# Optimization experiments

Hardware: AMD Instinct MI355X
Metric: run time of the kernel (lower is better)

Reference implementation:

```python
import jax, jax.numpy as jnp
import numpy as np

D_MODEL = 2048
N_HEADS = 16
HEAD_DIM = D_MODEL // N_HEADS
SEQ = 2048
THETA = 10000.0


def rope_tables(head_dim, context_length, theta=THETA):
    inv_freq = 1.0 / theta ** (jnp.arange(0, head_dim, 2, dtype=jnp.float32) / head_dim)
    angles = jnp.arange(context_length, dtype=jnp.float32)[:, None] * inv_freq[None, :]
    angles = jnp.concatenate([angles, angles], axis=1)  # [S, head_dim]
    return jnp.cos(angles), jnp.sin(angles)


def apply_rope(x, cos, sin):
    # x: [B, H, S, Dh]; cos/sin: [S, Dh]
    half = x.shape[-1] // 2
    x1, x2 = x[..., :half], x[..., half:]
    rotated = jnp.concatenate([-x2, x1], axis=-1)
    return x * cos[None, None] + rotated * sin[None, None]


def setup_inputs() -> dict:
    key = jax.random.key(0)
    ks = jax.random.split(key, 5)
    s = 1.0 / np.sqrt(D_MODEL)
    x = jax.random.normal(ks[0], (2, SEQ, D_MODEL), dtype=jnp.float32)
    Wq = jax.random.normal(ks[1], (D_MODEL, D_MODEL), dtype=jnp.float32) * s
    Wk = jax.random.normal(ks[2], (D_MODEL, D_MODEL), dtype=jnp.float32) * s
    Wv = jax.random.normal(ks[3], (D_MODEL, D_MODEL), dtype=jnp.float32) * s
    Wo = jax.random.normal(ks[4], (D_MODEL, D_MODEL), dtype=jnp.float32) * s
    return {"x": x, "Wq": Wq, "Wk": Wk, "Wv": Wv, "Wo": Wo}


def reference(x, Wq, Wk, Wv, Wo):
    B, S, D = x.shape
    cos, sin = rope_tables(HEAD_DIM, SEQ)
    cos, sin = cos[:S], sin[:S]

    def split_heads(t):  # [B,S,D] -> [B,H,S,Dh]
        return t.reshape(B, S, N_HEADS, HEAD_DIM).transpose(0, 2, 1, 3)

    q = apply_rope(split_heads(x @ Wq.T), cos, sin)
    k = apply_rope(split_heads(x @ Wk.T), cos, sin)
    v = split_heads(x @ Wv.T)

    scores = jnp.einsum('bhqd,bhkd->bhqk', q, k) / np.sqrt(HEAD_DIM).astype(np.float32)
    causal = jnp.tril(jnp.ones((S, S), dtype=bool))
    scores = jnp.where(causal[None, None], scores, -jnp.inf)
    weights = jax.nn.softmax(scores, axis=-1)
    ctx = jnp.einsum('bhqk,bhkd->bhqd', weights, v)
    ctx = ctx.transpose(0, 2, 1, 3).reshape(B, S, D)
    return ctx @ Wo.T
```

## Files before the change

kernel.cpp:

```cpp
#include <hip/hip_runtime.h>
#include <hip/hip_bf16.h>
#include <cstdint>
#include <cstddef>

typedef __bf16 bf16;
typedef __bf16 bf16x4 __attribute__((ext_vector_type(4)));
typedef __bf16 bf16x8 __attribute__((ext_vector_type(8)));
typedef float f32x4 __attribute__((ext_vector_type(4)));

#define D_MODEL 2048
#define SEQ     2048
#define NH      16
#define HD      128
#define BATCH   2
#define QKV_LD  6144

#define SBAR()  __builtin_amdgcn_sched_barrier(0)
#define HWBAR() do { SBAR(); __builtin_amdgcn_s_barrier(); SBAR(); } while (0)

__device__ __forceinline__ void gld16(void* lds, const void* g) {
    __builtin_amdgcn_global_load_lds(
        (const __attribute__((address_space(1))) unsigned int*)g,
        (__attribute__((address_space(3))) unsigned int*)lds,
        16, 0, 0);
}

__global__ __launch_bounds__(256) void cvt_all(const float* __restrict__ x,
                                               const float* __restrict__ Wq,
                                               const float* __restrict__ Wk,
                                               const float* __restrict__ Wv,
                                               const float* __restrict__ Wo,
                                               bf16* __restrict__ out) {
    int i = (blockIdx.x * 256 + threadIdx.x) * 4;
    const float* src;
    int off;
    if (i < 8388608) { src = x; off = i; }
    else {
        int j = i - 8388608;
        int seg = j >> 22;
        src = (seg == 0) ? Wq : (seg == 1) ? Wk : (seg == 2) ? Wv : Wo;
        off = j & 4194303;
    }
    float4 v = *(const float4*)(src + off);
    bf16* o = out + i;
    o[0] = (bf16)v.x; o[1] = (bf16)v.y; o[2] = (bf16)v.z; o[3] = (bf16)v.w;
}

__global__ __launch_bounds__(256) void rope_tables_k(float* __restrict__ cosd,
                                                     float* __restrict__ sind) {
    int id = blockIdx.x * 256 + threadIdx.x;
    int s = id >> 6, d = id & 63;
    float freq = powf(10000.f, -(float)d * (1.f / 64.f));
    float a = (float)s * freq;
    float sn, c;
    sincosf(a, &sn, &c);
    cosd[id] = c;
    sind[id] = sn;
}

__global__ __launch_bounds__(256) void rope_apply2(bf16* __restrict__ T,
                                                   const float* __restrict__ cosd,
                                                   const float* __restrict__ sind,
                                                   float qscale) {
    int id = blockIdx.x * 256 + threadIdx.x;
    int half = id >> 22;
    int jd = id & 4194303;
    int row = jd >> 10;
    int p = jd & 1023;
    int h = p >> 6, d = p & 63;
    int s = row & (SEQ - 1);
    size_t base = (size_t)row * QKV_LD + half * D_MODEL + h * HD + d;
    float scale = half ? 1.0f : qscale;
    float x1 = (float)T[base];
    float x2 = (float)T[base + 64];
    float c = cosd[(s << 6) + d];
    float sn = sind[(s << 6) + d];
    T[base]      = (bf16)((x1 * c - x2 * sn) * scale);
    T[base + 64] = (bf16)((x2 * c + x1 * sn) * scale);
}

__global__ __launch_bounds__(256) void transpose_v(const bf16* __restrict__ V,
                                                   bf16* __restrict__ Vt, int ld) {
    __shared__ bf16 t[32][33];
    int s0 = blockIdx.x * 32;
    int d0 = blockIdx.y * 32;
    int bh = blockIdx.z;
    int b = bh >> 4, h = bh & 15;
    int tx = threadIdx.x & 31, ty = threadIdx.x >> 5;
#pragma unroll
    for (int i = 0; i < 32; i += 8)
        t[ty + i][tx] = V[((size_t)(b * SEQ + s0 + ty + i)) * ld + h * HD + d0 + tx];
    __syncthreads();
#pragma unroll
    for (int i = 0; i < 32; i += 8)
        Vt[((size_t)bh * HD + d0 + ty + i) * SEQ + s0 + tx] = t[tx][ty + i];
}

template <int OUTF32>
__global__ __launch_bounds__(512, 2)
void gemm128(const bf16* __restrict__ A, const bf16* __restrict__ B,
             void* __restrict__ Cout, int M, int N, int K) {
    __shared__ __align__(16) bf16 ldsA[2][128 * 64];
    __shared__ __align__(16) bf16 ldsB[2][2][128 * 64];

    const int nN = N >> 8;
    const int cpx = gridDim.x >> 3;
    const int lin = (blockIdx.x & 7) * cpx + (blockIdx.x >> 3);
    const int m0 = (lin / nN) * 128, n0 = (lin % nN) * 256;

    const int tid = threadIdx.x;
    const int w = tid >> 6, l = tid & 63;
    const int wm = w >> 2, wn = w & 3;
    const int lg = l >> 4, lc = l & 15;
    const int swz = (lc & 7) << 4;
    const int NT = K >> 6;

    f32x4 acc[2][4][2] = {};

    auto stageA = [&](int tau) {
        bf16* dst = &ldsA[tau & 1][0];
#pragma unroll
        for (int j = 0; j < 2; ++j) {
            int r = w * 16 + j * 8 + (l >> 3);
            int scb = ((l & 7) * 16) ^ ((r & 7) << 4);
            gld16(dst + (w * 16 + j * 8) * 64, A + (size_t)(m0 + r) * K + tau * 64 + (scb >> 1));
        }
    };
    auto stageB = [&](int tau, int u) {
        bf16* dst = &ldsB[tau & 1][u][0];
#pragma unroll
        for (int j = 0; j < 2; ++j) {
            int r = w * 16 + j * 8 + (l >> 3);
            int scb = ((l & 7) * 16) ^ ((r & 7) << 4);
            gld16(dst + (w * 16 + j * 8) * 64, B + (size_t)(n0 + u * 128 + r) * K + tau * 64 + (scb >> 1));
        }
    };

    stageA(0); stageB(0, 0); stageB(0, 1); stageA(1);
    SBAR();
    asm volatile("s_waitcnt vmcnt(2)" ::: "memory");
    HWBAR();

    for (int t = 0; t < NT; ++t) {
        const int c = t & 1;
        const char* Ab = (const char*)&ldsA[c][0];
        const char* Bb = (const char*)&ldsB[c][wn >> 1][0];
        const int brow0 = (wn & 1) * 64;
        bf16x8 Af[4][2], Bf[2][2];

#pragma unroll
        for (int mt = 0; mt < 4; ++mt)
#pragma unroll
            for (int ks = 0; ks < 2; ++ks)
                Af[mt][ks] = *(const bf16x8*)(Ab + (wm * 64 + mt * 16 + lc) * 128 + ((ks * 64 + lg * 16) ^ swz));
#pragma unroll
        for (int nt = 0; nt < 2; ++nt)
#pragma unroll
            for (int ks = 0; ks < 2; ++ks)
                Bf[nt][ks] = *(const bf16x8*)(Bb + (brow0 + nt * 16 + lc) * 128 + ((ks * 64 + lg * 16) ^ swz));
        if (t + 1 < NT) stageB(t + 1, 0);
        HWBAR();
        __builtin_amdgcn_s_setprio(1);
#pragma unroll
        for (int mt = 0; mt < 4; ++mt)
#pragma unroll
            for (int nt = 0; nt < 2; ++nt)
#pragma unroll
                for (int ks = 0; ks < 2; ++ks)
                    acc[0][mt][nt] = __builtin_amdgcn_mfma_f32_16x16x32_bf16(Af[mt][ks], Bf[nt][ks], acc[0][mt][nt], 0, 0, 0);
        __builtin_amdgcn_s_setprio(0);
        HWBAR();

#pragma unroll
        for (int nt = 0; nt < 2; ++nt)
#pragma unroll
            for (int ks = 0; ks < 2; ++ks)
                Bf[nt][ks] = *(const bf16x8*)(Bb + (brow0 + 32 + nt * 16 + lc) * 128 + ((ks * 64 + lg * 16) ^ swz));
        if (t + 1 < NT) stageB(t + 1, 1);
        if (t + 2 < NT) stageA(t + 2);
        HWBAR();
        __builtin_amdgcn_s_setprio(1);
#pragma unroll
        for (int mt = 0; mt < 4; ++mt)
#pragma unroll
            for (int nt = 0; nt < 2; ++nt)
#pragma unroll
                for (int ks = 0; ks < 2; ++ks)
                    acc[1][mt][nt] = __builtin_amdgcn_mfma_f32_16x16x32_bf16(Af[mt][ks], Bf[nt][ks], acc[1][mt][nt], 0, 0, 0);
        __builtin_amdgcn_s_setprio(0);
        SBAR();
        if (t + 2 < NT) asm volatile("s_waitcnt vmcnt(2)" ::: "memory");
        else            asm volatile("s_waitcnt vmcnt(0)" ::: "memory");
        HWBAR();
    }

#pragma unroll
    for (int nq = 0; nq < 2; ++nq)
#pragma unroll
        for (int mt = 0; mt < 4; ++mt)
#pragma unroll
            for (int nt = 0; nt < 2; ++nt)
#pragma unroll
                for (int rr = 0; rr < 4; ++rr) {
                    size_t row = (size_t)m0 + wm * 64 + mt * 16 + lg * 4 + rr;
                    size_t col = (size_t)n0 + wn * 64 + nq * 32 + nt * 16 + lc;
                    float v = acc[nq][mt][nt][rr];
                    if (OUTF32) ((float*)Cout)[row * N + col] = v;
                    else        ((bf16*)Cout)[row * N + col] = (bf16)v;
                }
}

__global__ __launch_bounds__(512)
void flash_attn(const bf16* __restrict__ QKV, const bf16* __restrict__ Vt,
                bf16* __restrict__ O) {
    __shared__ __align__(16) bf16 Ks[2][64 * 128];
    __shared__ __align__(16) bf16 Vs[2][128 * 64];
    __shared__ __align__(16) bf16 p_lds[8][16 * 64];

    const int bid = blockIdx.x;
    const int xcd = bid & 7, loc = bid >> 3;
    const int bh = (xcd << 2) + (loc & 3);
    const int jjj = loc >> 2;
    const int qt = (jjj < 8) ? (15 - jjj) : (jjj - 8);
    const int b = bh >> 4, h = bh & 15;

    const int tid = threadIdx.x;
    const int w = tid >> 6, l = tid & 63;
    const int lg = l >> 4, lc = l & 15;
    const int kswz = (lc & 7) << 4;
    char* pb = (char*)&p_lds[w][0];

    auto stageK = [&](int p, int kb) {
#pragma unroll
        for (int c = 0; c < 2; ++c) {
            int r = c * 32 + w * 4 + (l >> 4);
            int scb = ((l & 15) * 16) ^ ((r & 7) << 4);
            const bf16* g = QKV + ((size_t)(b * SEQ + kb * 64 + r)) * QKV_LD + D_MODEL + h * HD + (scb >> 1);
            gld16(&Ks[p][(c * 32 + w * 4) * 128], g);
        }
    };
    auto stageV = [&](int p, int kb) {
#pragma unroll
        for (int c = 0; c < 2; ++c) {
            int r = c * 64 + w * 8 + (l >> 3);
            int scb = ((l & 7) * 16) ^ ((r & 7) << 4);
            const bf16* g = Vt + ((size_t)bh * HD + r) * SEQ + kb * 64 + (scb >> 1);
            gld16(&Vs[p][(c * 64 + w * 8) * 64], g);
        }
    };

    const int q0 = qt * 128 + w * 16;
    const int kbmax = 2 * qt + 1;

    const bf16* qp = QKV + ((size_t)(b * SEQ + q0 + lc)) * QKV_LD + h * HD + lg * 8;
    bf16x8 qf[4];
#pragma unroll
    for (int kc = 0; kc < 4; ++kc) qf[kc] = *(const bf16x8*)(qp + kc * 32);

    f32x4 ctx[8] = {};
    float m_s = -INFINITY, l_s = 0.f;

    int cur = 0;
    stageK(cur, 0);
    stageV(cur, 0);

    for (int kb = 0; kb <= kbmax; ++kb) {
        __syncthreads();
        if (kb < kbmax) { stageK(cur ^ 1, kb + 1); stageV(cur ^ 1, kb + 1); }

        const char* kbp = (const char*)&Ks[cur][0];
        f32x4 st[4] = {};
#pragma unroll
        for (int nf = 0; nf < 4; ++nf) {
            int krow = nf * 16 + lc;
#pragma unroll
            for (int kc = 0; kc < 4; ++kc) {
                bf16x8 kf = *(const bf16x8*)(kbp + krow * 256 + ((kc * 64 + lg * 16) ^ kswz));
                st[nf] = __builtin_amdgcn_mfma_f32_16x16x32_bf16(kf, qf[kc], st[nf], 0, 0, 0);
            }
        }

        if (kb >= 2 * qt) {
            int q = q0 + lc;
#pragma unroll
            for (int nf = 0; nf < 4; ++nf) {
                int key = kb * 64 + nf * 16 + lg * 4;
#pragma unroll
                for (int r = 0; r < 4; ++r)
                    if (key + r > q) st[nf][r] = -INFINITY;
            }
        }

        float m01 = fmaxf(fmaxf(st[0][0], st[0][1]), fmaxf(st[0][2], st[0][3]));
        float m23 = fmaxf(fmaxf(st[1][0], st[1][1]), fmaxf(st[1][2], st[1][3]));
        float m45 = fmaxf(fmaxf(st[2][0], st[2][1]), fmaxf(st[2][2], st[2][3]));
        float m67 = fmaxf(fmaxf(st[3][0], st[3][1]), fmaxf(st[3][2], st[3][3]));
        float mx = fmaxf(fmaxf(m01, m23), fmaxf(m45, m67));
        mx = fmaxf(mx, __shfl_xor(mx, 16));
        mx = fmaxf(mx, __shfl_xor(mx, 32));

        bool defer = __all(mx <= m_s + 8.f) && (m_s > -INFINITY);
        float mi;
        if (defer) {
            mi = m_s;
        } else {
            mi = fmaxf(m_s, mx);
            float scv = __expf(m_s - mi);
            float scvr[4];
#pragma unroll
            for (int r = 0; r < 4; ++r) scvr[r] = __shfl(scv, lg * 4 + r);
#pragma unroll
            for (int nd = 0; nd < 8; ++nd)
#pragma unroll
                for (int r = 0; r < 4; ++r) ctx[nd][r] *= scvr[r];
            l_s *= scv;
            m_s = mi;
        }

        float rs = 0.f;
#pragma unroll
        for (int nf = 0; nf < 4; ++nf) {
            float p0 = __expf(st[nf][0] - mi);
            float p1 = __expf(st[nf][1] - mi);
            float p2 = __expf(st[nf][2] - mi);
            float p3 = __expf(st[nf][3] - mi);
            rs += (p0 + p1) + (p2 + p3);
            bf16x4 pv = { (bf16)p0, (bf16)p1, (bf16)p2, (bf16)p3 };
            *(bf16x4*)(pb + lc * 128 + ((nf * 32 + lg * 8) ^ kswz)) = pv;
        }
        rs += __shfl_xor(rs, 16);
        rs += __shfl_xor(rs, 32);
        l_s += rs;

        asm volatile("s_waitcnt lgkmcnt(0)" ::: "memory");
        SBAR();
        bf16x8 pa0 = *(const bf16x8*)(pb + lc * 128 + ((lg * 16) ^ kswz));
        bf16x8 pa1 = *(const bf16x8*)(pb + lc * 128 + ((64 + lg * 16) ^ kswz));

        const char* vb = (const char*)&Vs[cur][0];
#pragma unroll
        for (int nd = 0; nd < 8; ++nd) {
            int vrow = nd * 16 + lc;
#pragma unroll
            for (int k2 = 0; k2 < 2; ++k2) {
                bf16x8 vf = *(const bf16x8*)(vb + vrow * 128 + ((k2 * 64 + lg * 16) ^ kswz));
                ctx[nd] = __builtin_amdgcn_mfma_f32_16x16x32_bf16(k2 ? pa1 : pa0, vf, ctx[nd], 0, 0, 0);
            }
        }
        cur ^= 1;
    }

    float lr[4];
#pragma unroll
    for (int r = 0; r < 4; ++r) lr[r] = 1.f / __shfl(l_s, lg * 4 + r);
#pragma unroll
    for (int nd = 0; nd < 8; ++nd)
#pragma unroll
        for (int r = 0; r < 4; ++r)
            O[((size_t)(b * SEQ + q0 + lg * 4 + r)) * D_MODEL + h * HD + nd * 16 + lc] =
                (bf16)(ctx[nd][r] * lr[r]);
}

extern "C" void kernel_launch(void* const* d_in, const int* in_sizes, int n_in,
                              void* d_out, int out_size, void* d_ws, size_t ws_size,
                              hipStream_t stream) {
    const float* x  = (const float*)d_in[0];
    const float* Wq = (const float*)d_in[1];
    const float* Wk = (const float*)d_in[2];
    const float* Wv = (const float*)d_in[3];
    const float* Wo = (const float*)d_in[4];

    char* ws = (char*)d_ws;
    bf16* xb   = (bf16*)(ws + 0);
    bf16* wqkv = (bf16*)(ws + 16777216);
    bf16* wob  = (bf16*)(ws + 41943040);
    bf16* QKV  = (bf16*)(ws + 50331648);
    bf16* Vtb  = (bf16*)(ws + 100663296);
    float* cosd = (float*)(ws + 117440512);
    float* sind = (float*)(ws + 117964800);

    cvt_all<<<25165824 / 1024, 256, 0, stream>>>(x, Wq, Wk, Wv, Wo, xb);

    rope_tables_k<<<(SEQ * 64) / 256, 256, 0, stream>>>(cosd, sind);

    gemm128<0><<<dim3(768), 512, 0, stream>>>(
        xb, wqkv, QKV, BATCH * SEQ, QKV_LD, D_MODEL);

    const float qscale = 0.08838834764831845f;
    rope_apply2<<<(2 * BATCH * SEQ * 1024) / 256, 256, 0, stream>>>(QKV, cosd, sind, qscale);

    transpose_v<<<dim3(SEQ / 32, HD / 32, BATCH * NH), 256, 0, stream>>>(QKV + 2 * D_MODEL, Vtb, QKV_LD);

    flash_attn<<<dim3(512), 512, 0, stream>>>(QKV, Vtb, xb );

    gemm128<1><<<dim3(256), 512, 0, stream>>>(
        xb, wob, d_out, BATCH * SEQ, D_MODEL, D_MODEL);
}
```

Before: 269.1 us.

## Use 256x256 tiled GEMM with quadrant-split pipeline for QKV projection

```diff
diff --git a/kernel.cpp b/kernel.cpp
--- a/kernel.cpp
+++ b/kernel.cpp
@@ -98,6 +98,147 @@
 
 template <int OUTF32>
 __global__ __launch_bounds__(512, 2)
+void gemm256(const bf16* __restrict__ A, const bf16* __restrict__ B,
+             void* __restrict__ Cout, int M, int N, int K) {
+    __shared__ __align__(16) bf16 lds[2][2][2][128 * 64];
+
+    const int nN = N >> 8;
+    const int cpx = gridDim.x >> 3;
+    const int lin = (blockIdx.x & 7) * cpx + (blockIdx.x >> 3);
+    const int m0 = (lin / nN) * 256, n0 = (lin % nN) * 256;
+
+    const int tid = threadIdx.x;
+    const int w = tid >> 6, l = tid & 63;
+    const int wm = w >> 2, wn = w & 3;
+    const int lg = l >> 4, lc = l & 15;
+    const int swz = (lc & 7) << 4;
+    const int NT = K >> 6;
+
+    f32x4 acc[2][2][4][2] = {};
+
+    auto stage = [&](int tau, int ab, int u) {
+        bf16* dst = &lds[tau & 1][ab][u][0];
+        const bf16* src = (ab == 0) ? A + (size_t)(m0 + u * 128) * K
+                                    : B + (size_t)(n0 + u * 128) * K;
+#pragma unroll
+        for (int j = 0; j < 2; ++j) {
+            int r = w * 16 + j * 8 + (l >> 3);
+            int scb = ((l & 7) * 16) ^ ((r & 7) << 4);
+            gld16(dst + (w * 16 + j * 8) * 64, src + (size_t)r * K + tau * 64 + (scb >> 1));
+        }
+    };
+
+    stage(0, 0, 0); stage(0, 0, 1); stage(0, 1, 0); stage(0, 1, 1);
+    stage(1, 1, 0); stage(1, 0, 0);
+    SBAR();
+    asm volatile("s_waitcnt vmcnt(4)" ::: "memory");
+    HWBAR();
+
+    for (int t = 0; t < NT; ++t) {
+        const char* Ab = (const char*)&lds[t & 1][0][wm][0];
+        const char* Bb = (const char*)&lds[t & 1][1][wn >> 1][0];
+        const int brow0 = (wn & 1) * 64;
+        bf16x8 Af[4][2], Bf[2][2][2];
+
+#pragma unroll
+        for (int mt = 0; mt < 4; ++mt)
+#pragma unroll
+            for (int ks = 0; ks < 2; ++ks)
+                Af[mt][ks] = *(const bf16x8*)(Ab + (mt * 16 + lc) * 128 + ((ks * 64 + lg * 16) ^ swz));
+#pragma unroll
+        for (int nt = 0; nt < 2; ++nt)
+#pragma unroll
+            for (int ks = 0; ks < 2; ++ks)
+                Bf[0][nt][ks] = *(const bf16x8*)(Bb + (brow0 + nt * 16 + lc) * 128 + ((ks * 64 + lg * 16) ^ swz));
+        if (t + 1 < NT) stage(t + 1, 1, 1);
+        SBAR(); __builtin_amdgcn_s_barrier();
+        asm volatile("s_waitcnt lgkmcnt(0)" ::: "memory"); SBAR();
+        __builtin_amdgcn_s_setprio(1);
+#pragma unroll
+        for (int mt = 0; mt < 4; ++mt)
+#pragma unroll
+            for (int nt = 0; nt < 2; ++nt)
+#pragma unroll
+                for (int ks = 0; ks < 2; ++ks)
+                    acc[0][0][mt][nt] = __builtin_amdgcn_mfma_f32_16x16x32_bf16(Af[mt][ks], Bf[0][nt][ks], acc[0][0][mt][nt], 0, 0, 0);
+        __builtin_amdgcn_s_setprio(0);
+        HWBAR();
+
+#pragma unroll
+        for (int nt = 0; nt < 2; ++nt)
+#pragma unroll
+            for (int ks = 0; ks < 2; ++ks)
+                Bf[1][nt][ks] = *(const bf16x8*)(Bb + (brow0 + 32 + nt * 16 + lc) * 128 + ((ks * 64 + lg * 16) ^ swz));
+        if (t + 1 < NT) stage(t + 1, 0, 1);
+        SBAR(); __builtin_amdgcn_s_barrier();
+        asm volatile("s_waitcnt lgkmcnt(0)" ::: "memory"); SBAR();
+        __builtin_amdgcn_s_setprio(1);
+#pragma unroll
+        for (int mt = 0; mt < 4; ++mt)
+#pragma unroll
+            for (int nt = 0; nt < 2; ++nt)
+#pragma unroll
+                for (int ks = 0; ks < 2; ++ks)
+                    acc[0][1][mt][nt] = __builtin_amdgcn_mfma_f32_16x16x32_bf16(Af[mt][ks], Bf[1][nt][ks], acc[0][1][mt][nt], 0, 0, 0);
+        __builtin_amdgcn_s_setprio(0);
+        HWBAR();
+
+#pragma unroll
+        for (int mt = 0; mt < 4; ++mt)
+#pragma unroll
+            for (int ks = 0; ks < 2; ++ks)
+                Af[mt][ks] = *(const bf16x8*)(Ab + (64 + mt * 16 + lc) * 128 + ((ks * 64 + lg * 16) ^ swz));
+        if (t + 2 < NT) stage(t + 2, 1, 0);
+        SBAR(); __builtin_amdgcn_s_barrier();
+        asm volatile("s_waitcnt lgkmcnt(0)" ::: "memory"); SBAR();
+        __builtin_amdgcn_s_setprio(1);
+#pragma unroll
+        for (int mt = 0; mt < 4; ++mt)
+#pragma unroll
+            for (int nt = 0; nt < 2; ++nt)
+#pragma unroll
+                for (int ks = 0; ks < 2; ++ks)
+                    acc[1][0][mt][nt] = __builtin_amdgcn_mfma_f32_16x16x32_bf16(Af[mt][ks], Bf[0][nt][ks], acc[1][0][mt][nt], 0, 0, 0);
+        __builtin_amdgcn_s_setprio(0);
+        HWBAR();
+
+        if (t + 2 < NT) stage(t + 2, 0, 0);
+        SBAR(); __builtin_amdgcn_s_barrier(); SBAR();
+        __builtin_amdgcn_s_setprio(1);
+#pragma unroll
+        for (int mt = 0; mt < 4; ++mt)
+#pragma unroll
+            for (int nt = 0; nt < 2; ++nt)
+#pragma unroll
+                for (int ks = 0; ks < 2; ++ks)
+                    acc[1][1][mt][nt] = __builtin_amdgcn_mfma_f32_16x16x32_bf16(Af[mt][ks], Bf[1][nt][ks], acc[1][1][mt][nt], 0, 0, 0);
+        __builtin_amdgcn_s_setprio(0);
+        SBAR();
+        if (t + 2 < NT) asm volatile("s_waitcnt vmcnt(4)" ::: "memory");
+        else            asm volatile("s_waitcnt vmcnt(0)" ::: "memory");
+        __builtin_amdgcn_s_barrier(); SBAR();
+    }
+
+#pragma unroll
+    for (int mq = 0; mq < 2; ++mq)
+#pragma unroll
+        for (int nq = 0; nq < 2; ++nq)
+#pragma unroll
+            for (int mt = 0; mt < 4; ++mt)
+#pragma unroll
+                for (int nt = 0; nt < 2; ++nt)
+#pragma unroll
+                    for (int rr = 0; rr < 4; ++rr) {
+                        size_t row = (size_t)m0 + wm * 128 + mq * 64 + mt * 16 + lg * 4 + rr;
+                        size_t col = (size_t)n0 + wn * 64 + nq * 32 + nt * 16 + lc;
+                        float v = acc[mq][nq][mt][nt][rr];
+                        if (OUTF32) ((float*)Cout)[row * N + col] = v;
+                        else        ((bf16*)Cout)[row * N + col] = (bf16)v;
+                    }
+}
+
+template <int OUTF32>
+__global__ __launch_bounds__(512, 2)
 void gemm128(const bf16* __restrict__ A, const bf16* __restrict__ B,
              void* __restrict__ Cout, int M, int N, int K) {
     __shared__ __align__(16) bf16 ldsA[2][128 * 64];
@@ -383,7 +524,7 @@
 
     rope_tables_k<<<(SEQ * 64) / 256, 256, 0, stream>>>(cosd, sind);
 
-    gemm128<0><<<dim3(768), 512, 0, stream>>>(
+    gemm256<0><<<dim3(384), 512, 0, stream>>>(
         xb, wqkv, QKV, BATCH * SEQ, QKV_LD, D_MODEL);
 
     const float qscale = 0.08838834764831845f;
```

Result: no change. 267.7 us (-0.5%).
